# Kernel tuning notes

Measured on AMD Instinct MI355X. Metric: run time of the kernel, lower is better.

## Reference

```python
import jax, jax.numpy as jnp
import numpy as np

H = 1024      # hidden size (n_embd)
F = 4 * H     # ffn hidden
E = 8         # num experts
K = 2         # top_k


def setup_inputs() -> dict:
    key = jax.random.key(0)
    ks = jax.random.split(key, 6)
    s = 1.0 / np.sqrt(H)
    sf = 1.0 / np.sqrt(F)
    return {
        "x": jax.random.normal(ks[0], (2, 2048, H), dtype=jnp.float32),
        "w_gate": jax.random.uniform(ks[1], (H, E), minval=-s, maxval=s, dtype=jnp.float32),
        "w_fc": jax.random.uniform(ks[2], (E, H, F), minval=-s, maxval=s, dtype=jnp.float32),
        "b_fc": jnp.zeros((E, F), dtype=jnp.float32),
        "w_proj": jax.random.uniform(ks[3], (E, F, H), minval=-sf, maxval=sf, dtype=jnp.float32),
        "b_proj": jnp.zeros((E, H), dtype=jnp.float32),
    }


def reference(x, w_gate, w_fc, b_fc, w_proj, b_proj):
    B, S, Hh = x.shape
    T = B * S
    x_flat = x.reshape(T, Hh)

    # --- Router ---
    logits = x_flat @ w_gate                       # (T, E)
    probs = jax.nn.softmax(logits, axis=-1)
    topk_w, topk_idx = jax.lax.top_k(probs, K)     # (T, K)
    topk_w = topk_w / (jnp.sum(topk_w, axis=-1, keepdims=True) + 1e-9)

    # Aux load-balancing loss (Switch style, top-1 counts)
    top1 = topk_idx[:, 0]
    tokens_per_expert = jax.ops.segment_sum(jnp.ones((T,), x.dtype), top1, num_segments=E)
    f = tokens_per_expert / T
    P = probs.mean(axis=0)
    aux_loss = E * jnp.sum(f * P)

    # Per-token per-expert combine weights (0 for non-selected experts)
    cw = jnp.zeros((T, E), x.dtype).at[jnp.arange(T)[:, None], topk_idx].add(topk_w)  # (T, E)

    # --- Experts (dense batched FFN, masked combine — same math as gather/scatter loop) ---
    h = jnp.einsum('th,ehf->etf', x_flat, w_fc) + b_fc[:, None, :]   # (E, T, F)
    h = jax.nn.gelu(h, approximate=False)
    y = jnp.einsum('etf,efh->eth', h, w_proj) + b_proj[:, None, :]   # (E, T, H)
    out = jnp.einsum('eth,te->th', y, cw)                            # (T, H)

    return out.reshape(B, S, Hh), aux_loss
```

## Files before the change

### kernel.cpp

```cpp
#include <hip/hip_runtime.h>
#include <hip/hip_bf16.h>
#include <math.h>

#define Hdim 1024
#define Fdim 4096
#define NE   8
#define TOPK 2
#define NT   4096
#define NASSIGN (NT*TOPK)

typedef __bf16 bf16x8 __attribute__((ext_vector_type(8)));
typedef __bf16 bf16x4 __attribute__((ext_vector_type(4)));
typedef float  floatx4 __attribute__((ext_vector_type(4)));

__device__ __forceinline__ void ld16_lds(const void* g, void* l) {
  __builtin_amdgcn_global_load_lds(
      (const __attribute__((address_space(1))) void*)g,
      (__attribute__((address_space(3))) void*)l,
      16, 0, 0);
}

__global__ void xcvt_kernel(const float* __restrict__ x, __bf16* __restrict__ Xb) {
  int i = blockIdx.x * 256 + threadIdx.x;
  float4 v = ((const float4*)x)[i];
  bf16x4 o;
  o[0] = (__bf16)v.x; o[1] = (__bf16)v.y; o[2] = (__bf16)v.z; o[3] = (__bf16)v.w;
  ((bf16x4*)Xb)[i] = o;
}

__global__ void transpose_cvt_kernel(const float* __restrict__ W,
                                     __bf16* __restrict__ Wt,
                                     int Kd, int Nd) {
  __shared__ float tile[64][65];
  int e  = blockIdx.z;
  int n0 = blockIdx.x * 64;
  int k0 = blockIdx.y * 64;
  const float* We  = W  + (size_t)e * Kd * Nd;
  __bf16*      Wte = Wt + (size_t)e * Kd * Nd;
  int tx = threadIdx.x & 63, ty = threadIdx.x >> 6;
  #pragma unroll
  for (int r = ty; r < 64; r += 4)
    tile[r][tx] = We[(size_t)(k0 + r) * Nd + n0 + tx];
  __syncthreads();
  #pragma unroll
  for (int r = ty; r < 64; r += 4)
    Wte[(size_t)(n0 + r) * Kd + k0 + tx] = (__bf16)tile[tx][r];
}

__global__ void gating_kernel(const float* __restrict__ x,
                              const float* __restrict__ wg,
                              int* __restrict__ topk_idx,
                              float* __restrict__ topk_w,
                              float* __restrict__ probs) {
  int w = threadIdx.x >> 6, l = threadIdx.x & 63;
  int t = blockIdx.x * 4 + w;
  const float* xr = x + (size_t)t * Hdim;
  float acc[NE];
  #pragma unroll
  for (int e = 0; e < NE; ++e) acc[e] = 0.f;
  #pragma unroll
  for (int j = 0; j < Hdim / 64; ++j) {
    int h = j * 64 + l;
    float xv = xr[h];
    const float* wr = wg + h * NE;
    #pragma unroll
    for (int e = 0; e < NE; ++e) acc[e] += xv * wr[e];
  }
  #pragma unroll
  for (int off = 32; off; off >>= 1)
    #pragma unroll
    for (int e = 0; e < NE; ++e) acc[e] += __shfl_xor(acc[e], off, 64);
  if (l == 0) {
    float m = acc[0];
    #pragma unroll
    for (int e = 1; e < NE; ++e) m = fmaxf(m, acc[e]);
    float p[NE], s = 0.f;
    #pragma unroll
    for (int e = 0; e < NE; ++e) { p[e] = expf(acc[e] - m); s += p[e]; }
    float inv = 1.f / s;
    #pragma unroll
    for (int e = 0; e < NE; ++e) p[e] *= inv;
    int e0 = 0; float b0 = p[0];
    #pragma unroll
    for (int e = 1; e < NE; ++e) if (p[e] > b0) { b0 = p[e]; e0 = e; }
    int e1 = (e0 == 0) ? 1 : 0; float b1 = p[e1];
    #pragma unroll
    for (int e = 0; e < NE; ++e)
      if (e != e0 && p[e] > b1) { b1 = p[e]; e1 = e; }
    float s2 = b0 + b1 + 1e-9f;
    topk_idx[t * 2] = e0; topk_idx[t * 2 + 1] = e1;
    topk_w[t * 2] = b0 / s2; topk_w[t * 2 + 1] = b1 / s2;
    #pragma unroll
    for (int e = 0; e < NE; ++e) probs[t * NE + e] = p[e];
  }
}

__global__ void reduce_kernel(const int* __restrict__ topk_idx,
                              const float* __restrict__ probs,
                              int* __restrict__ acnt,
                              int* __restrict__ aoff,
                              int* __restrict__ fill,
                              float* __restrict__ out_aux) {
  __shared__ int s_acnt[NE];
  __shared__ int s_cnt1[NE];
  __shared__ float s_psum[NE];
  int tid = threadIdx.x;
  if (tid < NE) { s_acnt[tid] = 0; s_cnt1[tid] = 0; s_psum[tid] = 0.f; }
  __syncthreads();
  int c_a[NE], c_1[NE];
  float c_p[NE];
  #pragma unroll
  for (int e = 0; e < NE; ++e) { c_a[e] = 0; c_1[e] = 0; c_p[e] = 0.f; }
  for (int t = tid; t < NT; t += 256) {
    int e0 = topk_idx[t * 2], e1 = topk_idx[t * 2 + 1];
    #pragma unroll
    for (int e = 0; e < NE; ++e) {
      c_a[e] += (e == e0) + (e == e1);
      c_1[e] += (e == e0);
      c_p[e] += probs[t * NE + e];
    }
  }
  #pragma unroll
  for (int e = 0; e < NE; ++e) {
    atomicAdd(&s_acnt[e], c_a[e]);
    atomicAdd(&s_cnt1[e], c_1[e]);
    atomicAdd(&s_psum[e], c_p[e]);
  }
  __syncthreads();
  if (tid == 0) {
    int o = 0; float aux = 0.f;
    for (int e = 0; e < NE; ++e) {
      acnt[e] = s_acnt[e];
      aoff[e] = o; fill[e] = o; o += s_acnt[e];
      aux += ((float)s_cnt1[e] / (float)NT) * (s_psum[e] / (float)NT);
    }
    out_aux[0] = (float)NE * aux;
  }
}

__global__ void scatter_kernel(const int* __restrict__ topk_idx,
                               const float* __restrict__ topk_w,
                               int* __restrict__ fill,
                               int* __restrict__ token_map,
                               float* __restrict__ weight_map) {
  __shared__ int s_cnt[NE];
  __shared__ int s_base[NE];
  int tid = threadIdx.x;
  if (tid < NE) s_cnt[tid] = 0;
  __syncthreads();
  int t = blockIdx.x * 256 + tid;
  int e0 = topk_idx[t * 2], e1 = topk_idx[t * 2 + 1];
  int r0 = atomicAdd(&s_cnt[e0], 1);
  int r1 = atomicAdd(&s_cnt[e1], 1);
  __syncthreads();
  if (tid < NE) s_base[tid] = atomicAdd(&fill[tid], s_cnt[tid]);
  __syncthreads();
  int slot0 = s_base[e0] + r0;
  int slot1 = s_base[e1] + r1;
  token_map[slot0] = t; weight_map[slot0] = topk_w[t * 2];
  token_map[slot1] = t; weight_map[slot1] = topk_w[t * 2 + 1];
}

template <int KD, int ND, int MODE>
__launch_bounds__(256)
__global__ void moe_gemm_kernel(const __bf16* __restrict__ Abase,
                                const __bf16* __restrict__ Wt,
                                const float* __restrict__ bias,
                                const int* __restrict__ acnt,
                                const int* __restrict__ aoff,
                                const int* __restrict__ token_map,
                                const float* __restrict__ weight_map,
                                __bf16* __restrict__ Hout,
                                float* __restrict__ out) {
  __shared__ __bf16 As[128 * 32];
  __shared__ __bf16 Bs[128 * 32];
  const int e = blockIdx.z;
  const int cnt = acnt[e];
  const int row0 = blockIdx.y * 128;
  if (row0 >= cnt) return;
  const int off = aoff[e];
  const int n0 = blockIdx.x * 128;
  const int tid = threadIdx.x;
  const int w = tid >> 6, l = tid & 63;
  const int arow = tid >> 2;
  const int acol = (tid & 3) * 8;

  const __bf16* gB0 = Wt + (size_t)e * ((size_t)ND * KD) + (size_t)(n0 + arow) * KD + acol;
  const __bf16* gB1 = gB0 + (size_t)64 * KD;
  const __bf16* gA0;
  const __bf16* gA1;
  if (MODE == 0) {
    int r0 = off + row0 + arow;
    int r1 = r0 + 64;
    int t0 = token_map[r0 < NASSIGN ? r0 : NASSIGN - 1];
    int t1 = token_map[r1 < NASSIGN ? r1 : NASSIGN - 1];
    gA0 = Abase + (size_t)t0 * KD + acol;
    gA1 = Abase + (size_t)t1 * KD + acol;
  } else {
    gA0 = Abase + (size_t)(off + row0 + arow) * KD + acol;
    gA1 = gA0 + (size_t)64 * KD;
  }

  floatx4 acc[4][4];
  {
    floatx4 z = {0.f, 0.f, 0.f, 0.f};
    #pragma unroll
    for (int i = 0; i < 4; ++i)
      #pragma unroll
      for (int j = 0; j < 4; ++j) acc[i][j] = z;
  }

  __bf16* lA = As + w * 512;
  __bf16* lB = Bs + w * 512;
  const int wr = (w >> 1) * 64, wc = (w & 1) * 64;
  const int lrow = l & 15, lq = l >> 4;

  for (int kt = 0; kt < KD; kt += 32) {
    __syncthreads();
    ld16_lds(gA0 + kt, lA);
    ld16_lds(gA1 + kt, lA + 2048);
    ld16_lds(gB0 + kt, lB);
    ld16_lds(gB1 + kt, lB + 2048);
    __syncthreads();
    bf16x8 af[4], bf[4];
    #pragma unroll
    for (int s = 0; s < 4; ++s) {
      af[s] = *(const bf16x8*)(As + (wr + s * 16 + lrow) * 32 + lq * 8);
      bf[s] = *(const bf16x8*)(Bs + (wc + s * 16 + lrow) * 32 + lq * 8);
    }
    #pragma unroll
    for (int sm = 0; sm < 4; ++sm)
      #pragma unroll
      for (int sn = 0; sn < 4; ++sn)
        acc[sm][sn] = __builtin_amdgcn_mfma_f32_16x16x32_bf16(af[sm], bf[sn], acc[sm][sn], 0, 0, 0);
  }

  #pragma unroll
  for (int sm = 0; sm < 4; ++sm) {
    int rowb = row0 + wr + sm * 16 + lq * 4;
    #pragma unroll
    for (int r = 0; r < 4; ++r) {
      int row = rowb + r;
      if (row < cnt) {
        if (MODE == 0) {
          size_t orow = (size_t)(off + row) * ND;
          #pragma unroll
          for (int sn = 0; sn < 4; ++sn) {
            int n = n0 + wc + sn * 16 + lrow;
            float v = acc[sm][sn][r] + bias[e * ND + n];
            v = 0.5f * v * (1.0f + erff(v * 0.70710678118654752f));
            Hout[orow + n] = (__bf16)v;
          }
        } else {
          int s = off + row;
          int t = token_map[s];
          float wgt = weight_map[s];
          size_t obase = (size_t)t * ND;
          #pragma unroll
          for (int sn = 0; sn < 4; ++sn) {
            int n = n0 + wc + sn * 16 + lrow;
            float v = acc[sm][sn][r] + bias[e * ND + n];
            atomicAdd(&out[obase + n], wgt * v);
          }
        }
      }
    }
  }
}

extern "C" void kernel_launch(void* const* d_in, const int* in_sizes, int n_in,
                              void* d_out, int out_size, void* d_ws, size_t ws_size,
                              hipStream_t stream) {
  const float* x      = (const float*)d_in[0];
  const float* w_gate = (const float*)d_in[1];
  const float* w_fc   = (const float*)d_in[2];
  const float* b_fc   = (const float*)d_in[3];
  const float* w_proj = (const float*)d_in[4];
  const float* b_proj = (const float*)d_in[5];
  float* out = (float*)d_out;

  char* ws = (char*)d_ws;
  __bf16* Wfct   = (__bf16*)(ws);
  __bf16* Wprojt = (__bf16*)(ws + 67108864);
  __bf16* Xb     = (__bf16*)(ws + 134217728);
  __bf16* Hbuf   = (__bf16*)(ws + 142606336);
  char* tail = ws + 142606336 + (size_t)(NASSIGN + 128) * Fdim * 2;
  int*   token_map  = (int*)tail;
  float* weight_map = (float*)(tail + 32768);
  int*   topk_idx   = (int*)(tail + 65536);
  float* topk_w     = (float*)(tail + 98304);
  int*   cntrs      = (int*)(tail + 131072);
  int*   acnt = cntrs + 0;
  int*   aoff = cntrs + 16;
  int*   fill = cntrs + 24;
  float* probs      = (float*)(tail + 131072 + 256);

  hipMemsetAsync(d_out, 0, (size_t)out_size * sizeof(float), stream);

  xcvt_kernel<<<(NT * Hdim) / (256 * 4), 256, 0, stream>>>(x, Xb);
  transpose_cvt_kernel<<<dim3(Fdim / 64, Hdim / 64, NE), 256, 0, stream>>>(w_fc, Wfct, Hdim, Fdim);
  transpose_cvt_kernel<<<dim3(Hdim / 64, Fdim / 64, NE), 256, 0, stream>>>(w_proj, Wprojt, Fdim, Hdim);

  gating_kernel<<<NT / 4, 256, 0, stream>>>(x, w_gate, topk_idx, topk_w, probs);
  reduce_kernel<<<1, 256, 0, stream>>>(topk_idx, probs, acnt, aoff, fill,
                                       out + (size_t)NT * Hdim);
  scatter_kernel<<<NT / 256, 256, 0, stream>>>(topk_idx, topk_w, fill, token_map, weight_map);

  moe_gemm_kernel<Hdim, Fdim, 0><<<dim3(Fdim / 128, 32, NE), 256, 0, stream>>>(
      Xb, Wfct, b_fc, acnt, aoff, token_map, weight_map, Hbuf, out);
  moe_gemm_kernel<Fdim, Hdim, 1><<<dim3(Hdim / 128, 32, NE), 256, 0, stream>>>(
      Hbuf, Wprojt, b_proj, acnt, aoff, token_map, weight_map, (__bf16*)nullptr, out);

  (void)in_sizes; (void)n_in; (void)ws_size;
}
```

Before: 695.5 us.

## Split-K second GEMM, deterministic combine, LDS swizzle, tanh GELU, vectorized transpose

The second expert GEMM is split along K into two parts. Each part writes its unweighted partial outputs to a per-slot fp32 buffer, and a new combine kernel gathers the partials per token and applies the bias and routing weights. This replaces the atomic scatter-add and the output memset. The change also XOR-swizzles LDS columns in the GEMM to cut bank conflicts, vectorizes the weight transpose/convert kernel, and swaps the erf GELU for a tanh approximation, which changes numerics slightly. The workspace is re-laid out so the Y buffer aliases Xb and Wfct, which are dead by the time Y is written.

Result: faster. 669.0 us (-3.8%).

```diff
diff --git a/kernel.cpp b/kernel.cpp
--- a/kernel.cpp
+++ b/kernel.cpp
@@ -8,6 +8,7 @@
 #define TOPK 2
 #define NT   4096
 #define NASSIGN (NT*TOPK)
+#define YROWS (NASSIGN+128)
 
 typedef __bf16 bf16x8 __attribute__((ext_vector_type(8)));
 typedef __bf16 bf16x4 __attribute__((ext_vector_type(4)));
@@ -18,6 +19,13 @@
       (const __attribute__((address_space(1))) void*)g,
       (__attribute__((address_space(3))) void*)l,
       16, 0, 0);
+}
+
+__device__ __forceinline__ float gelu_f(float v) {
+  float u = 0.7978845608028654f * (v + 0.044715f * v * v * v);
+  float ex = __expf(2.0f * u);
+  float th = 1.0f - 2.0f / (ex + 1.0f);
+  return 0.5f * v * (1.0f + th);
 }
 
 __global__ void xcvt_kernel(const float* __restrict__ x, __bf16* __restrict__ Xb) {
@@ -37,14 +45,26 @@
   int k0 = blockIdx.y * 64;
   const float* We  = W  + (size_t)e * Kd * Nd;
   __bf16*      Wte = Wt + (size_t)e * Kd * Nd;
-  int tx = threadIdx.x & 63, ty = threadIdx.x >> 6;
-  #pragma unroll
-  for (int r = ty; r < 64; r += 4)
-    tile[r][tx] = We[(size_t)(k0 + r) * Nd + n0 + tx];
-  __syncthreads();
-  #pragma unroll
-  for (int r = ty; r < 64; r += 4)
-    Wte[(size_t)(n0 + r) * Kd + k0 + tx] = (__bf16)tile[tx][r];
+  int tid = threadIdx.x;
+  int r = tid >> 4, c4 = (tid & 15) * 4;
+  #pragma unroll
+  for (int p = 0; p < 4; ++p) {
+    float4 v = *(const float4*)(We + (size_t)(k0 + p * 16 + r) * Nd + n0 + c4);
+    tile[p * 16 + r][c4]     = v.x;
+    tile[p * 16 + r][c4 + 1] = v.y;
+    tile[p * 16 + r][c4 + 2] = v.z;
+    tile[p * 16 + r][c4 + 3] = v.w;
+  }
+  __syncthreads();
+  int n = tid >> 3, k8 = (tid & 7) * 8;
+  #pragma unroll
+  for (int p = 0; p < 2; ++p) {
+    int nn = p * 32 + n;
+    bf16x8 o;
+    #pragma unroll
+    for (int j = 0; j < 8; ++j) o[j] = (__bf16)tile[k8 + j][nn];
+    *(bf16x8*)(Wte + (size_t)(n0 + nn) * Kd + k0 + k8) = o;
+  }
 }
 
 __global__ void gating_kernel(const float* __restrict__ x,
@@ -139,10 +159,9 @@
 }
 
 __global__ void scatter_kernel(const int* __restrict__ topk_idx,
-                               const float* __restrict__ topk_w,
                                int* __restrict__ fill,
                                int* __restrict__ token_map,
-                               float* __restrict__ weight_map) {
+                               int* __restrict__ islot) {
   __shared__ int s_cnt[NE];
   __shared__ int s_base[NE];
   int tid = threadIdx.x;
@@ -157,11 +176,13 @@
   __syncthreads();
   int slot0 = s_base[e0] + r0;
   int slot1 = s_base[e1] + r1;
-  token_map[slot0] = t; weight_map[slot0] = topk_w[t * 2];
-  token_map[slot1] = t; weight_map[slot1] = topk_w[t * 2 + 1];
-}
-
-template <int KD, int ND, int MODE>
+  token_map[slot0] = t;
+  token_map[slot1] = t;
+  islot[t * 2] = slot0;
+  islot[t * 2 + 1] = slot1;
+}
+
+template <int KD, int ND, int MODE, int KPARTS>
 __launch_bounds__(256)
 __global__ void moe_gemm_kernel(const __bf16* __restrict__ Abase,
                                 const __bf16* __restrict__ Wt,
@@ -169,9 +190,8 @@
                                 const int* __restrict__ acnt,
                                 const int* __restrict__ aoff,
                                 const int* __restrict__ token_map,
-                                const float* __restrict__ weight_map,
                                 __bf16* __restrict__ Hout,
-                                float* __restrict__ out) {
+                                float* __restrict__ Yout) {
   __shared__ __bf16 As[128 * 32];
   __shared__ __bf16 Bs[128 * 32];
   const int e = blockIdx.z;
@@ -179,13 +199,16 @@
   const int row0 = blockIdx.y * 128;
   if (row0 >= cnt) return;
   const int off = aoff[e];
-  const int n0 = blockIdx.x * 128;
+  const int part  = (KPARTS > 1) ? (int)(blockIdx.x & (KPARTS - 1)) : 0;
+  const int n0    = ((KPARTS > 1) ? (int)(blockIdx.x >> 1) : (int)blockIdx.x) * 128;
+  const int kbase = part * (KD / KPARTS);
+  constexpr int KLEN = KD / KPARTS;
   const int tid = threadIdx.x;
   const int w = tid >> 6, l = tid & 63;
   const int arow = tid >> 2;
-  const int acol = (tid & 3) * 8;
-
-  const __bf16* gB0 = Wt + (size_t)e * ((size_t)ND * KD) + (size_t)(n0 + arow) * KD + acol;
+  const int acol = (((tid & 3) ^ ((arow >> 1) & 3)) * 8);
+
+  const __bf16* gB0 = Wt + (size_t)e * ((size_t)ND * KD) + (size_t)(n0 + arow) * KD + kbase + acol;
   const __bf16* gB1 = gB0 + (size_t)64 * KD;
   const __bf16* gA0;
   const __bf16* gA1;
@@ -194,10 +217,10 @@
     int r1 = r0 + 64;
     int t0 = token_map[r0 < NASSIGN ? r0 : NASSIGN - 1];
     int t1 = token_map[r1 < NASSIGN ? r1 : NASSIGN - 1];
-    gA0 = Abase + (size_t)t0 * KD + acol;
-    gA1 = Abase + (size_t)t1 * KD + acol;
+    gA0 = Abase + (size_t)t0 * KD + kbase + acol;
+    gA1 = Abase + (size_t)t1 * KD + kbase + acol;
   } else {
-    gA0 = Abase + (size_t)(off + row0 + arow) * KD + acol;
+    gA0 = Abase + (size_t)(off + row0 + arow) * KD + kbase + acol;
     gA1 = gA0 + (size_t)64 * KD;
   }
 
@@ -214,8 +237,9 @@
   __bf16* lB = Bs + w * 512;
   const int wr = (w >> 1) * 64, wc = (w & 1) * 64;
   const int lrow = l & 15, lq = l >> 4;
-
-  for (int kt = 0; kt < KD; kt += 32) {
+  const int ck8 = (lq ^ ((lrow >> 1) & 3)) * 8;
+
+  for (int kt = 0; kt < KLEN; kt += 32) {
     __syncthreads();
     ld16_lds(gA0 + kt, lA);
     ld16_lds(gA1 + kt, lA + 2048);
@@ -225,8 +249,8 @@
     bf16x8 af[4], bf[4];
     #pragma unroll
     for (int s = 0; s < 4; ++s) {
-      af[s] = *(const bf16x8*)(As + (wr + s * 16 + lrow) * 32 + lq * 8);
-      bf[s] = *(const bf16x8*)(Bs + (wc + s * 16 + lrow) * 32 + lq * 8);
+      af[s] = *(const bf16x8*)(As + (wr + s * 16 + lrow) * 32 + ck8);
+      bf[s] = *(const bf16x8*)(Bs + (wc + s * 16 + lrow) * 32 + ck8);
     }
     #pragma unroll
     for (int sm = 0; sm < 4; ++sm)
@@ -235,6 +259,7 @@
         acc[sm][sn] = __builtin_amdgcn_mfma_f32_16x16x32_bf16(af[sm], bf[sn], acc[sm][sn], 0, 0, 0);
   }
 
+  float* yp = (MODE == 1) ? (Yout + (size_t)part * ((size_t)YROWS * ND)) : nullptr;
   #pragma unroll
   for (int sm = 0; sm < 4; ++sm) {
     int rowb = row0 + wr + sm * 16 + lq * 4;
@@ -248,24 +273,45 @@
           for (int sn = 0; sn < 4; ++sn) {
             int n = n0 + wc + sn * 16 + lrow;
             float v = acc[sm][sn][r] + bias[e * ND + n];
-            v = 0.5f * v * (1.0f + erff(v * 0.70710678118654752f));
-            Hout[orow + n] = (__bf16)v;
+            Hout[orow + n] = (__bf16)gelu_f(v);
           }
         } else {
-          int s = off + row;
-          int t = token_map[s];
-          float wgt = weight_map[s];
-          size_t obase = (size_t)t * ND;
+          size_t orow = (size_t)(off + row) * ND;
           #pragma unroll
           for (int sn = 0; sn < 4; ++sn) {
             int n = n0 + wc + sn * 16 + lrow;
-            float v = acc[sm][sn][r] + bias[e * ND + n];
-            atomicAdd(&out[obase + n], wgt * v);
+            yp[orow + n] = acc[sm][sn][r];
           }
         }
       }
     }
   }
+}
+
+__global__ void combine_kernel(const float* __restrict__ Y,
+                               const int* __restrict__ topk_idx,
+                               const float* __restrict__ topk_w,
+                               const int* __restrict__ islot,
+                               const float* __restrict__ b_proj,
+                               float* __restrict__ out) {
+  int t = blockIdx.x, tid = threadIdx.x;
+  int s0 = islot[t * 2], s1 = islot[t * 2 + 1];
+  int e0 = topk_idx[t * 2], e1 = topk_idx[t * 2 + 1];
+  float w0 = topk_w[t * 2], w1 = topk_w[t * 2 + 1];
+  const float4* Y0 = (const float4*)Y;
+  const float4* Y1 = (const float4*)(Y + (size_t)YROWS * Hdim);
+  float4 a0 = Y0[(size_t)s0 * 256 + tid];
+  float4 a1 = Y1[(size_t)s0 * 256 + tid];
+  float4 c0 = Y0[(size_t)s1 * 256 + tid];
+  float4 c1 = Y1[(size_t)s1 * 256 + tid];
+  float4 b0 = ((const float4*)(b_proj + (size_t)e0 * Hdim))[tid];
+  float4 b1 = ((const float4*)(b_proj + (size_t)e1 * Hdim))[tid];
+  float4 o;
+  o.x = w0 * (a0.x + a1.x + b0.x) + w1 * (c0.x + c1.x + b1.x);
+  o.y = w0 * (a0.y + a1.y + b0.y) + w1 * (c0.y + c1.y + b1.y);
+  o.z = w0 * (a0.z + a1.z + b0.z) + w1 * (c0.z + c1.z + b1.z);
+  o.w = w0 * (a0.w + a1.w + b0.w) + w1 * (c0.w + c1.w + b1.w);
+  ((float4*)(out + (size_t)t * Hdim))[tid] = o;
 }
 
 extern "C" void kernel_launch(void* const* d_in, const int* in_sizes, int n_in,
@@ -280,13 +326,14 @@
   float* out = (float*)d_out;
 
   char* ws = (char*)d_ws;
-  __bf16* Wfct   = (__bf16*)(ws);
-  __bf16* Wprojt = (__bf16*)(ws + 67108864);
-  __bf16* Xb     = (__bf16*)(ws + 134217728);
+  __bf16* Xb     = (__bf16*)(ws);
+  __bf16* Wfct   = (__bf16*)(ws + 8388608);
+  float*  Ybuf   = (float*)(ws);
+  __bf16* Wprojt = (__bf16*)(ws + 75497472);
   __bf16* Hbuf   = (__bf16*)(ws + 142606336);
-  char* tail = ws + 142606336 + (size_t)(NASSIGN + 128) * Fdim * 2;
+  char* tail = ws + 142606336 + (size_t)YROWS * Fdim * 2;
   int*   token_map  = (int*)tail;
-  float* weight_map = (float*)(tail + 32768);
+  int*   islot      = (int*)(tail + 32768);
   int*   topk_idx   = (int*)(tail + 65536);
   float* topk_w     = (float*)(tail + 98304);
   int*   cntrs      = (int*)(tail + 131072);
@@ -295,8 +342,6 @@
   int*   fill = cntrs + 24;
   float* probs      = (float*)(tail + 131072 + 256);
 
-  hipMemsetAsync(d_out, 0, (size_t)out_size * sizeof(float), stream);
-
   xcvt_kernel<<<(NT * Hdim) / (256 * 4), 256, 0, stream>>>(x, Xb);
   transpose_cvt_kernel<<<dim3(Fdim / 64, Hdim / 64, NE), 256, 0, stream>>>(w_fc, Wfct, Hdim, Fdim);
   transpose_cvt_kernel<<<dim3(Hdim / 64, Fdim / 64, NE), 256, 0, stream>>>(w_proj, Wprojt, Fdim, Hdim);
@@ -304,12 +349,14 @@
   gating_kernel<<<NT / 4, 256, 0, stream>>>(x, w_gate, topk_idx, topk_w, probs);
   reduce_kernel<<<1, 256, 0, stream>>>(topk_idx, probs, acnt, aoff, fill,
                                        out + (size_t)NT * Hdim);
-  scatter_kernel<<<NT / 256, 256, 0, stream>>>(topk_idx, topk_w, fill, token_map, weight_map);
-
-  moe_gemm_kernel<Hdim, Fdim, 0><<<dim3(Fdim / 128, 32, NE), 256, 0, stream>>>(
-      Xb, Wfct, b_fc, acnt, aoff, token_map, weight_map, Hbuf, out);
-  moe_gemm_kernel<Fdim, Hdim, 1><<<dim3(Hdim / 128, 32, NE), 256, 0, stream>>>(
-      Hbuf, Wprojt, b_proj, acnt, aoff, token_map, weight_map, (__bf16*)nullptr, out);
+  scatter_kernel<<<NT / 256, 256, 0, stream>>>(topk_idx, fill, token_map, islot);
+
+  moe_gemm_kernel<Hdim, Fdim, 0, 1><<<dim3(Fdim / 128, 32, NE), 256, 0, stream>>>(
+      Xb, Wfct, b_fc, acnt, aoff, token_map, Hbuf, nullptr);
+  moe_gemm_kernel<Fdim, Hdim, 1, 2><<<dim3((Hdim / 128) * 2, 32, NE), 256, 0, stream>>>(
+      Hbuf, Wprojt, nullptr, acnt, aoff, token_map, nullptr, Ybuf);
+
+  combine_kernel<<<NT, 256, 0, stream>>>(Ybuf, topk_idx, topk_w, islot, b_proj, out);
 
   (void)in_sizes; (void)n_in; (void)ws_size;
 }
```
